# Performance work log

Hardware: AMD Instinct MI355X
Metric: run time of the kernel (lower is better)

Reference implementation:

```python
import jax, jax.numpy as jnp
import numpy as np

EMBED_DIM = 256
MAX_SENT_NUM = 50


def position_embeddings(max_sent_num, embed_dim):
    # pos[p, i] = sin(p / 200**(i/embed_dim))
    p = jnp.arange(max_sent_num, dtype=jnp.float32)[:, None]
    i = jnp.arange(embed_dim, dtype=jnp.float32)[None, :] / embed_dim
    return jnp.sin(p / jnp.power(200.0, i))


def setup_inputs() -> dict:
    key = jax.random.key(0)
    k1, k2, k3, k4 = jax.random.split(key, 4)
    B, S, N, E = 8192, 50, 20, EMBED_DIM
    return {
        "encoded_sents": jax.random.normal(k1, (B, S, E), dtype=jnp.float32),
        "entities": jax.random.normal(k2, (B, N, E), dtype=jnp.float32),
        "attn_matrix": jax.random.normal(k3, (E, E), dtype=jnp.float32) * 0.05,
        "dense_w": jax.random.normal(k4, (E, 1), dtype=jnp.float32) * 0.05,
        "dense_b": jnp.zeros((1,), dtype=jnp.float32),
    }


def reference(encoded_sents, entities, attn_matrix, dense_w, dense_b):
    B, S, E = encoded_sents.shape
    pos = position_embeddings(MAX_SENT_NUM, E)[:S]          # [S, E]
    x = encoded_sents + pos[None, :, :]                      # [B, S, E]

    # attention over previous sentences; query = last sentence's hidden state
    query = x[:, -1, :]                                      # [B, E]
    logits = jnp.einsum("be,bse->bs", query, x)              # [B, S]
    coef = jax.nn.softmax(logits, axis=1)                    # [B, S]
    attn_hidden = jnp.einsum("bs,bse->be", coef, x)          # [B, E]

    # entity attention: (query @ W) elementwise-weighted sum over entities (no softmax)
    q_ent = attn_hidden @ attn_matrix                        # [B, E]
    attn_ent = jnp.einsum("be,bne->be", q_ent, entities)     # [B, E] (sum over n)

    return jax.nn.sigmoid(attn_ent @ dense_w + dense_b)      # [B, 1]
```

## Files before the change

kernel.cpp:

```cpp
#include <hip/hip_runtime.h>
#include <math.h>

#define BATCH 8192
#define SENTS 50
#define ED    256
#define NENT  20
#define BB    16

#define RATE_K 0.0298588132413075f

__global__ __launch_bounds__(256) void pos_kernel(float* __restrict__ pos_tab) {
    int s = blockIdx.x;
    int e = threadIdx.x;
    float rate = exp2f(-(float)e * RATE_K);
    pos_tab[s * ED + e] = sinf((float)s * rate);
}

__global__ __launch_bounds__(256) void main_kernel(
    const float* __restrict__ sents, const float* __restrict__ entities,
    const float* __restrict__ dense_w, const float* __restrict__ pos_tab,
    float* __restrict__ h_out, float* __restrict__ m_out)
{
    __shared__ float logit_s[64];
    __shared__ float coef[64];
    __shared__ __align__(16) float4 part[4][64];
    __shared__ __align__(16) float4 parte[4][64];

    int t  = threadIdx.x;
    int b  = blockIdx.x;
    int c  = t & 63;
    int sr = t >> 6;

    const float4* s4 = (const float4*)(sents + (size_t)b * SENTS * ED);
    const float4* p4 = (const float4*)pos_tab;
    const float4* e4 = (const float4*)(entities + (size_t)b * NENT * ED);

    bool has13 = (sr < 2);

    float4 xv[13], pv[13], ev[5];
    #pragma unroll
    for (int k = 0; k < 12; ++k) xv[k] = s4[(sr + 4 * k) * 64 + c];
    float4 qsv = s4[49 * 64 + c];
    float4 qpv = p4[49 * 64 + c];
    #pragma unroll
    for (int k = 0; k < 12; ++k) pv[k] = p4[(sr + 4 * k) * 64 + c];
    #pragma unroll
    for (int n = 0; n < 5; ++n) ev[n] = e4[(sr + 4 * n) * 64 + c];
    if (has13) {
        xv[12] = s4[(sr + 48) * 64 + c];
        pv[12] = p4[(sr + 48) * 64 + c];
    }

    float4 x[13];
    #pragma unroll
    for (int k = 0; k < 12; ++k) {
        x[k].x = xv[k].x + pv[k].x; x[k].y = xv[k].y + pv[k].y;
        x[k].z = xv[k].z + pv[k].z; x[k].w = xv[k].w + pv[k].w;
    }
    if (has13) {
        x[12].x = xv[12].x + pv[12].x; x[12].y = xv[12].y + pv[12].y;
        x[12].z = xv[12].z + pv[12].z; x[12].w = xv[12].w + pv[12].w;
    } else {
        x[12] = make_float4(0.f, 0.f, 0.f, 0.f);
    }
    float4 q;
    q.x = qsv.x + qpv.x; q.y = qsv.y + qpv.y;
    q.z = qsv.z + qpv.z; q.w = qsv.w + qpv.w;

    float4 es = make_float4(0.f, 0.f, 0.f, 0.f);
    #pragma unroll
    for (int n = 0; n < 5; ++n) {
        es.x += ev[n].x; es.y += ev[n].y; es.z += ev[n].z; es.w += ev[n].w;
    }

    #pragma unroll
    for (int k = 0; k < 13; ++k) {
        if (k < 12 || has13) {
            float4 v = x[k];
            float p = v.x * q.x + v.y * q.y + v.z * q.z + v.w * q.w;
            p += __shfl_down(p, 32);
            p += __shfl_down(p, 16);
            p += __shfl_down(p, 8);
            p += __shfl_down(p, 4);
            p += __shfl_down(p, 2);
            p += __shfl_down(p, 1);
            if (c == 0) logit_s[sr + 4 * k] = p;
        }
    }
    __syncthreads();

    if (sr == 0) {
        float l = (c < SENTS) ? logit_s[c] : -INFINITY;
        float mx = l;
        for (int off = 32; off >= 1; off >>= 1) mx = fmaxf(mx, __shfl_xor(mx, off));
        float ex = (c < SENTS) ? expf(l - mx) : 0.f;
        float sm = ex;
        for (int off = 32; off >= 1; off >>= 1) sm += __shfl_xor(sm, off);
        if (c < SENTS) coef[c] = ex / sm;
    }
    __syncthreads();

    float4 h = make_float4(0.f, 0.f, 0.f, 0.f);
    #pragma unroll
    for (int k = 0; k < 13; ++k) {
        if (k < 12 || has13) {
            float cf = coef[sr + 4 * k];
            h.x += cf * x[k].x; h.y += cf * x[k].y;
            h.z += cf * x[k].z; h.w += cf * x[k].w;
        }
    }
    part[sr][c]  = h;
    parte[sr][c] = es;
    __syncthreads();

    if (sr == 0) {
        float4 a0 = part[0][c], a1 = part[1][c], a2 = part[2][c], a3 = part[3][c];
        float4 r;
        r.x = a0.x + a1.x + a2.x + a3.x;
        r.y = a0.y + a1.y + a2.y + a3.y;
        r.z = a0.z + a1.z + a2.z + a3.z;
        r.w = a0.w + a1.w + a2.w + a3.w;
        ((float4*)(h_out + (size_t)b * ED))[c] = r;
    } else if (sr == 1) {
        float4 a0 = parte[0][c], a1 = parte[1][c], a2 = parte[2][c], a3 = parte[3][c];
        float4 w4 = ((const float4*)dense_w)[c];
        float4 r;
        r.x = (a0.x + a1.x + a2.x + a3.x) * w4.x;
        r.y = (a0.y + a1.y + a2.y + a3.y) * w4.y;
        r.z = (a0.z + a1.z + a2.z + a3.z) * w4.z;
        r.w = (a0.w + a1.w + a2.w + a3.w) * w4.w;
        ((float4*)(m_out + (size_t)b * ED))[c] = r;
    }
}

__global__ __launch_bounds__(256) void bilinear_kernel(
    const float* __restrict__ hws, const float* __restrict__ mws,
    const float* __restrict__ A, const float* __restrict__ dense_b,
    float* __restrict__ out)
{
    __shared__ __align__(16) float hl[BB][ED];
    __shared__ float ml[BB][ED];
    __shared__ float part[BB][ED];

    int t  = threadIdx.x;
    int b0 = blockIdx.x * BB;

    for (int i = 0; i < BB; ++i) {
        hl[i][t] = hws[(size_t)(b0 + i) * ED + t];
        ml[i][t] = mws[(size_t)(b0 + i) * ED + t];
    }
    __syncthreads();

    float acc[BB];
    #pragma unroll
    for (int i = 0; i < BB; ++i) acc[i] = 0.f;

    for (int ep = 0; ep < ED; ep += 4) {
        float a0 = A[(ep + 0) * ED + t];
        float a1 = A[(ep + 1) * ED + t];
        float a2 = A[(ep + 2) * ED + t];
        float a3 = A[(ep + 3) * ED + t];
        #pragma unroll
        for (int i = 0; i < BB; ++i) {
            float4 hv = *(const float4*)&hl[i][ep];
            acc[i] += hv.x * a0 + hv.y * a1 + hv.z * a2 + hv.w * a3;
        }
    }

    #pragma unroll
    for (int i = 0; i < BB; ++i) part[i][t] = acc[i] * ml[i][t];
    __syncthreads();

    int lane = t & 63, w = t >> 6;
    float bias = dense_b[0];
    for (int i = w; i < BB; i += 4) {
        float v = part[i][lane] + part[i][lane + 64] + part[i][lane + 128] + part[i][lane + 192];
        for (int off = 32; off >= 1; off >>= 1) v += __shfl_xor(v, off);
        if (lane == 0) out[b0 + i] = 1.f / (1.f + expf(-(v + bias)));
    }
}

__global__ __launch_bounds__(256) void fused_kernel(
    const float* __restrict__ sents, const float* __restrict__ entities,
    const float* __restrict__ A, const float* __restrict__ dense_w,
    const float* __restrict__ dense_b, float* __restrict__ out)
{
    __shared__ __align__(16) float xs[SENTS][ED + 4];
    __shared__ float logit_s[64];
    __shared__ float coef[64];
    __shared__ __align__(16) float harr[ED];
    __shared__ float marr[ED];
    __shared__ float red[4];

    int t    = threadIdx.x;
    int b    = blockIdx.x;
    int lane = t & 63;
    int w    = t >> 6;

    float rate = exp2f(-(float)t * RATE_K);
    const float* sp = sents + (size_t)b * SENTS * ED;
    for (int s = 0; s < SENTS; ++s)
        xs[s][t] = sp[s * ED + t] + sinf((float)s * rate);
    __syncthreads();

    float4 q = *(const float4*)&xs[SENTS - 1][lane * 4];
    for (int s = w; s < SENTS; s += 4) {
        float4 v = *(const float4*)&xs[s][lane * 4];
        float p = v.x * q.x + v.y * q.y + v.z * q.z + v.w * q.w;
        p += __shfl_down(p, 32);
        p += __shfl_down(p, 16);
        p += __shfl_down(p, 8);
        p += __shfl_down(p, 4);
        p += __shfl_down(p, 2);
        p += __shfl_down(p, 1);
        if (lane == 0) logit_s[s] = p;
    }
    __syncthreads();

    if (w == 0) {
        float l = (lane < SENTS) ? logit_s[lane] : -INFINITY;
        float mx = l;
        for (int off = 32; off >= 1; off >>= 1) mx = fmaxf(mx, __shfl_xor(mx, off));
        float ex = (lane < SENTS) ? expf(l - mx) : 0.f;
        float sm = ex;
        for (int off = 32; off >= 1; off >>= 1) sm += __shfl_xor(sm, off);
        if (lane < SENTS) coef[lane] = ex / sm;
    }
    __syncthreads();

    float h = 0.f;
    #pragma unroll
    for (int s = 0; s < SENTS; ++s) h += coef[s] * xs[s][t];

    const float* ent = entities + (size_t)b * NENT * ED;
    float es = 0.f;
    #pragma unroll
    for (int n = 0; n < NENT; ++n) es += ent[n * ED + t];
    float m = es * dense_w[t];

    harr[t] = h;
    marr[t] = m;
    __syncthreads();

    float acc = 0.f;
    for (int ep = 0; ep < ED; ep += 4) {
        float4 hv = *(const float4*)&harr[ep];
        acc += hv.x * A[(ep + 0) * ED + t];
        acc += hv.y * A[(ep + 1) * ED + t];
        acc += hv.z * A[(ep + 2) * ED + t];
        acc += hv.w * A[(ep + 3) * ED + t];
    }
    float val = acc * marr[t];
    val += __shfl_down(val, 32);
    val += __shfl_down(val, 16);
    val += __shfl_down(val, 8);
    val += __shfl_down(val, 4);
    val += __shfl_down(val, 2);
    val += __shfl_down(val, 1);
    if (lane == 0) red[w] = val;
    __syncthreads();
    if (t == 0) {
        float tot = red[0] + red[1] + red[2] + red[3];
        out[b] = 1.f / (1.f + expf(-(tot + dense_b[0])));
    }
}

extern "C" void kernel_launch(void* const* d_in, const int* in_sizes, int n_in,
                              void* d_out, int out_size, void* d_ws, size_t ws_size,
                              hipStream_t stream) {
    const float* sents    = (const float*)d_in[0];
    const float* entities = (const float*)d_in[1];
    const float* A        = (const float*)d_in[2];
    const float* dense_w  = (const float*)d_in[3];
    const float* dense_b  = (const float*)d_in[4];
    float* out = (float*)d_out;

    size_t pos_bytes = (size_t)SENTS * ED * sizeof(float);
    size_t hm_bytes  = (size_t)BATCH * ED * sizeof(float);
    size_t need = pos_bytes + 2 * hm_bytes;

    if (ws_size >= need) {
        float* pos_tab = (float*)d_ws;
        float* hws = (float*)((char*)d_ws + pos_bytes);
        float* mws = (float*)((char*)d_ws + pos_bytes + hm_bytes);
        pos_kernel<<<SENTS, ED, 0, stream>>>(pos_tab);
        main_kernel<<<BATCH, 256, 0, stream>>>(sents, entities, dense_w, pos_tab, hws, mws);
        bilinear_kernel<<<BATCH / BB, 256, 0, stream>>>(hws, mws, A, dense_b, out);
    } else {
        fused_kernel<<<BATCH, 256, 0, stream>>>(sents, entities, A, dense_w, dense_b, out);
    }
}
```

Measured before the change: 162.1 us.

## Split entity sum into separate kernel and widen attention blocks to 512 threads

Moves the per-batch entity summation and dense_w scaling out of the attention kernel into its own kernel, where each 256-thread block covers four batch rows with 20 loads per thread. The attention kernel now runs 512 threads per batch row, with 8 sentence rows per group instead of 4, so each thread holds fewer registers and more memory-level parallelism is exposed. The aim is to raise occupancy and bandwidth use on a memory-bound workload. The cost is one extra kernel launch, and the launches run in series rather than overlapping the two independent reads.

```diff
diff --git a/kernel.cpp b/kernel.cpp
--- a/kernel.cpp
+++ b/kernel.cpp
@@ -16,15 +16,38 @@
     pos_tab[s * ED + e] = sinf((float)s * rate);
 }
 
-__global__ __launch_bounds__(256) void main_kernel(
-    const float* __restrict__ sents, const float* __restrict__ entities,
-    const float* __restrict__ dense_w, const float* __restrict__ pos_tab,
-    float* __restrict__ h_out, float* __restrict__ m_out)
+__global__ __launch_bounds__(256) void ent_kernel(
+    const float* __restrict__ entities, const float* __restrict__ dense_w,
+    float* __restrict__ m_out)
+{
+    int t = threadIdx.x;
+    int b = blockIdx.x * 4 + (t >> 6);
+    int c = t & 63;
+
+    const float4* e4 = (const float4*)(entities + (size_t)b * NENT * ED);
+
+    float4 a[NENT];
+    #pragma unroll
+    for (int n = 0; n < NENT; ++n) a[n] = e4[n * 64 + c];
+
+    float4 s = make_float4(0.f, 0.f, 0.f, 0.f);
+    #pragma unroll
+    for (int n = 0; n < NENT; ++n) {
+        s.x += a[n].x; s.y += a[n].y; s.z += a[n].z; s.w += a[n].w;
+    }
+
+    float4 w4 = ((const float4*)dense_w)[c];
+    s.x *= w4.x; s.y *= w4.y; s.z *= w4.z; s.w *= w4.w;
+    ((float4*)(m_out + (size_t)b * ED))[c] = s;
+}
+
+__global__ __launch_bounds__(512) void attn_kernel(
+    const float* __restrict__ sents, const float* __restrict__ pos_tab,
+    float* __restrict__ h_out)
 {
     __shared__ float logit_s[64];
     __shared__ float coef[64];
-    __shared__ __align__(16) float4 part[4][64];
-    __shared__ __align__(16) float4 parte[4][64];
+    __shared__ __align__(16) float4 part[8][64];
 
     int t  = threadIdx.x;
     int b  = blockIdx.x;
@@ -33,49 +56,40 @@
 
     const float4* s4 = (const float4*)(sents + (size_t)b * SENTS * ED);
     const float4* p4 = (const float4*)pos_tab;
-    const float4* e4 = (const float4*)(entities + (size_t)b * NENT * ED);
-
-    bool has13 = (sr < 2);
-
-    float4 xv[13], pv[13], ev[5];
-    #pragma unroll
-    for (int k = 0; k < 12; ++k) xv[k] = s4[(sr + 4 * k) * 64 + c];
+
+    bool has7 = (sr < 2);
+
+    float4 xv[7], pv[7];
+    #pragma unroll
+    for (int k = 0; k < 6; ++k) xv[k] = s4[(sr + 8 * k) * 64 + c];
     float4 qsv = s4[49 * 64 + c];
+    #pragma unroll
+    for (int k = 0; k < 6; ++k) pv[k] = p4[(sr + 8 * k) * 64 + c];
     float4 qpv = p4[49 * 64 + c];
-    #pragma unroll
-    for (int k = 0; k < 12; ++k) pv[k] = p4[(sr + 4 * k) * 64 + c];
-    #pragma unroll
-    for (int n = 0; n < 5; ++n) ev[n] = e4[(sr + 4 * n) * 64 + c];
-    if (has13) {
-        xv[12] = s4[(sr + 48) * 64 + c];
-        pv[12] = p4[(sr + 48) * 64 + c];
-    }
-
-    float4 x[13];
-    #pragma unroll
-    for (int k = 0; k < 12; ++k) {
+    if (has7) {
+        xv[6] = s4[(sr + 48) * 64 + c];
+        pv[6] = p4[(sr + 48) * 64 + c];
+    }
+
+    float4 x[7];
+    #pragma unroll
+    for (int k = 0; k < 6; ++k) {
         x[k].x = xv[k].x + pv[k].x; x[k].y = xv[k].y + pv[k].y;
         x[k].z = xv[k].z + pv[k].z; x[k].w = xv[k].w + pv[k].w;
     }
-    if (has13) {
-        x[12].x = xv[12].x + pv[12].x; x[12].y = xv[12].y + pv[12].y;
-        x[12].z = xv[12].z + pv[12].z; x[12].w = xv[12].w + pv[12].w;
+    if (has7) {
+        x[6].x = xv[6].x + pv[6].x; x[6].y = xv[6].y + pv[6].y;
+        x[6].z = xv[6].z + pv[6].z; x[6].w = xv[6].w + pv[6].w;
     } else {
-        x[12] = make_float4(0.f, 0.f, 0.f, 0.f);
+        x[6] = make_float4(0.f, 0.f, 0.f, 0.f);
     }
     float4 q;
     q.x = qsv.x + qpv.x; q.y = qsv.y + qpv.y;
     q.z = qsv.z + qpv.z; q.w = qsv.w + qpv.w;
 
-    float4 es = make_float4(0.f, 0.f, 0.f, 0.f);
-    #pragma unroll
-    for (int n = 0; n < 5; ++n) {
-        es.x += ev[n].x; es.y += ev[n].y; es.z += ev[n].z; es.w += ev[n].w;
-    }
-
-    #pragma unroll
-    for (int k = 0; k < 13; ++k) {
-        if (k < 12 || has13) {
+    #pragma unroll
+    for (int k = 0; k < 7; ++k) {
+        if (k < 6 || has7) {
             float4 v = x[k];
             float p = v.x * q.x + v.y * q.y + v.z * q.z + v.w * q.w;
             p += __shfl_down(p, 32);
@@ -84,7 +98,7 @@
             p += __shfl_down(p, 4);
             p += __shfl_down(p, 2);
             p += __shfl_down(p, 1);
-            if (c == 0) logit_s[sr + 4 * k] = p;
+            if (c == 0) logit_s[sr + 8 * k] = p;
         }
     }
     __syncthreads();
@@ -102,34 +116,24 @@
 
     float4 h = make_float4(0.f, 0.f, 0.f, 0.f);
     #pragma unroll
-    for (int k = 0; k < 13; ++k) {
-        if (k < 12 || has13) {
-            float cf = coef[sr + 4 * k];
+    for (int k = 0; k < 7; ++k) {
+        if (k < 6 || has7) {
+            float cf = coef[sr + 8 * k];
             h.x += cf * x[k].x; h.y += cf * x[k].y;
             h.z += cf * x[k].z; h.w += cf * x[k].w;
         }
     }
-    part[sr][c]  = h;
-    parte[sr][c] = es;
+    part[sr][c] = h;
     __syncthreads();
 
     if (sr == 0) {
-        float4 a0 = part[0][c], a1 = part[1][c], a2 = part[2][c], a3 = part[3][c];
-        float4 r;
-        r.x = a0.x + a1.x + a2.x + a3.x;
-        r.y = a0.y + a1.y + a2.y + a3.y;
-        r.z = a0.z + a1.z + a2.z + a3.z;
-        r.w = a0.w + a1.w + a2.w + a3.w;
+        float4 r = make_float4(0.f, 0.f, 0.f, 0.f);
+        #pragma unroll
+        for (int i = 0; i < 8; ++i) {
+            float4 a = part[i][c];
+            r.x += a.x; r.y += a.y; r.z += a.z; r.w += a.w;
+        }
         ((float4*)(h_out + (size_t)b * ED))[c] = r;
-    } else if (sr == 1) {
-        float4 a0 = parte[0][c], a1 = parte[1][c], a2 = parte[2][c], a3 = parte[3][c];
-        float4 w4 = ((const float4*)dense_w)[c];
-        float4 r;
-        r.x = (a0.x + a1.x + a2.x + a3.x) * w4.x;
-        r.y = (a0.y + a1.y + a2.y + a3.y) * w4.y;
-        r.z = (a0.z + a1.z + a2.z + a3.z) * w4.z;
-        r.w = (a0.w + a1.w + a2.w + a3.w) * w4.w;
-        ((float4*)(m_out + (size_t)b * ED))[c] = r;
     }
 }
 
@@ -284,7 +288,8 @@
         float* hws = (float*)((char*)d_ws + pos_bytes);
         float* mws = (float*)((char*)d_ws + pos_bytes + hm_bytes);
         pos_kernel<<<SENTS, ED, 0, stream>>>(pos_tab);
-        main_kernel<<<BATCH, 256, 0, stream>>>(sents, entities, dense_w, pos_tab, hws, mws);
+        ent_kernel<<<BATCH / 4, 256, 0, stream>>>(entities, dense_w, mws);
+        attn_kernel<<<BATCH, 512, 0, stream>>>(sents, pos_tab, hws);
         bilinear_kernel<<<BATCH / BB, 256, 0, stream>>>(hws, mws, A, dense_b, out);
     } else {
         fused_kernel<<<BATCH, 256, 0, stream>>>(sents, entities, A, dense_w, dense_b, out);
```

After: 161.1 us. Within noise of the previous version (-0.6%).
